# Kernel optimization log

Hardware: AMD Instinct MI355X
Metric: run time of the kernel (lower is better)

## Reference

```python
import jax, jax.numpy as jnp
import numpy as np

C = 256
G = min(C // 4, 32)  # GroupNorm groups = 32
EPS = 1e-6


def group_norm(x, gamma, beta):
    B, Cc, H, W = x.shape
    xg = x.reshape(B, G, Cc // G, H, W)
    mean = xg.mean(axis=(2, 3, 4), keepdims=True)
    var = xg.var(axis=(2, 3, 4), keepdims=True)
    xg = (xg - mean) / jnp.sqrt(var + EPS)
    x = xg.reshape(B, Cc, H, W)
    return x * gamma[None, :, None, None] + beta[None, :, None, None]


def nin(h, W_, b_):
    # 1x1 conv as channel contraction: [B,C,H,W] x [C,D] -> [B,D,H,W]
    return jnp.einsum('bchw,cd->bdhw', h, W_) + b_[None, :, None, None]


def setup_inputs() -> dict:
    key = jax.random.key(0)
    ks = jax.random.split(key, 12)
    B, H, Wd = 4, 64, 64
    x = jax.random.normal(ks[0], (B, C, H, Wd), dtype=jnp.float32)
    gn_gamma = jnp.ones((C,), jnp.float32)
    gn_beta = jnp.zeros((C,), jnp.float32)
    scale = 0.1
    w0 = jax.random.normal(ks[1], (C, C), jnp.float32) * scale
    b0 = jnp.zeros((C,), jnp.float32)
    w1 = jax.random.normal(ks[2], (C, C), jnp.float32) * scale
    b1 = jnp.zeros((C,), jnp.float32)
    w2 = jax.random.normal(ks[3], (C, C), jnp.float32) * scale
    b2 = jnp.zeros((C,), jnp.float32)
    w3 = jax.random.normal(ks[4], (C, C), jnp.float32) * scale
    b3 = jnp.zeros((C,), jnp.float32)
    return {"x": x, "gn_gamma": gn_gamma, "gn_beta": gn_beta,
            "w0": w0, "b0": b0, "w1": w1, "b1": b1,
            "w2": w2, "b2": b2, "w3": w3, "b3": b3}


def reference(x, gn_gamma, gn_beta, w0, b0, w1, b1, w2, b2, w3, b3):
    B, Cc, H, Wd = x.shape
    h = group_norm(x, gn_gamma, gn_beta)
    q = nin(h, w0, b0)
    k = nin(h, w1, b1)
    v = nin(h, w2, b2)
    # attention over all spatial positions; scores [B,H,W,H,W]
    w = jnp.einsum('bchw,bcij->bhwij', q, k) * (Cc ** -0.5)
    w = jax.nn.softmax(w.reshape(B, H, Wd, H * Wd), axis=-1)
    w = w.reshape(B, H, Wd, H, Wd)
    h = jnp.einsum('bhwij,bcij->bchw', w, v)
    h = nin(h, w3, b3)
    return x + h  # skip_rescale=False
```

## Files before the change

kernel.cpp:

```cpp
#include <hip/hip_runtime.h>
#include <math.h>


typedef short short8    __attribute__((ext_vector_type(8)));
typedef ushort ushort8  __attribute__((ext_vector_type(8)));
typedef ushort ushort4v __attribute__((ext_vector_type(4)));
typedef float f32x4     __attribute__((ext_vector_type(4)));
typedef float f32x16    __attribute__((ext_vector_type(16)));

#define BB 4
#define CCH 256
#define NSP 4096
#define TEN ((size_t)BB * NSP * CCH)

__device__ __forceinline__ float b2f(ushort h){
  unsigned int u = ((unsigned int)h) << 16;
  float f; __builtin_memcpy(&f, &u, 4); return f;
}
__device__ __forceinline__ ushort f2b(float f){
  unsigned int u; __builtin_memcpy(&u, &f, 4);
  u += 0x7fffu + ((u >> 16) & 1u);
  return (ushort)(u >> 16);
}
__device__ __forceinline__ unsigned int pk2(float a, float b){
  unsigned int r;
  asm("v_cvt_pk_bf16_f32 %0, %1, %2" : "=&v"(r) : "v"(a), "v"(b));
  return r;
}
__device__ __forceinline__ void dma16(const void* g, void* l){
  __builtin_amdgcn_global_load_lds((const __attribute__((address_space(1))) void*)g,
                                   (__attribute__((address_space(3))) void*)l,
                                   16, 0, 0);
}

__global__ __launch_bounds__(256) void pre_k(const float* __restrict__ x,
                                             const float* __restrict__ w0,
                                             const float* __restrict__ w1,
                                             const float* __restrict__ w2,
                                             const float* __restrict__ w3,
                                             ushort* __restrict__ wT,
                                             float* __restrict__ sums){
  __shared__ ushort tile[64][72];
  __shared__ float red[8];
  const int bxx = blockIdx.x;
  const int t = threadIdx.x;
  if (bxx < 64){
    const int wsel = bxx >> 4, tb = bxx & 15;
    const float* w = (wsel==0) ? w0 : (wsel==1) ? w1 : (wsel==2) ? w2 : w3;
    ushort* dst = wT + (size_t)wsel * 65536;
    const int r0 = (tb >> 2) * 64, c0 = (tb & 3) * 64;
    #pragma unroll
    for (int p = 0; p < 2; p++){
      const int r = p*32 + (t >> 3), cc = (t & 7)*8;
      const float* wr = w + (size_t)(r0 + r)*256 + c0 + cc;
      f32x4 a = *(const f32x4*)wr;
      f32x4 d = *(const f32x4*)(wr + 4);
      #pragma unroll
      for (int j = 0; j < 4; j++){
        tile[r][cc + j]     = f2b(a[j]);
        tile[r][cc + 4 + j] = f2b(d[j]);
      }
    }
    __syncthreads();
    #pragma unroll
    for (int p = 0; p < 2; p++){
      const int r = p*32 + (t >> 3), cc = (t & 7)*8;
      ushort8 ov;
      #pragma unroll
      for (int j = 0; j < 8; j++) ov[j] = tile[cc + j][r];
      *(ushort8*)(dst + (size_t)(c0 + r)*256 + r0 + cc) = ov;
    }
  } else {
    const int q = bxx - 64;
    const f32x4* p = (const f32x4*)(x + (size_t)(q >> 1)*32768 + (size_t)(q & 1)*16384);
    float s = 0.f, s2 = 0.f;
    for (int i = t; i < 4096; i += 256){
      f32x4 v = p[i];
      #pragma unroll
      for (int j = 0; j < 4; j++){ s += v[j]; s2 += v[j]*v[j]; }
    }
    #pragma unroll
    for (int off = 32; off >= 1; off >>= 1){
      s  += __shfl_down(s,  off, 64);
      s2 += __shfl_down(s2, off, 64);
    }
    const int w = t >> 6;
    if ((t & 63) == 0){ red[w*2] = s; red[w*2+1] = s2; }
    __syncthreads();
    if (t == 0){
      sums[q*2]   = red[0]+red[2]+red[4]+red[6];
      sums[q*2+1] = red[1]+red[3]+red[5]+red[7];
    }
  }
}

__global__ __launch_bounds__(256) void gn_apply_k(const float* __restrict__ x,
                                                  const float* __restrict__ sums,
                                                  const float* __restrict__ gamma,
                                                  const float* __restrict__ beta,
                                                  ushort* __restrict__ h_t){
  __shared__ ushort tile[64][72];
  const int b = blockIdx.z, c0 = blockIdx.y*64, n0 = blockIdx.x*64;
  const int t = threadIdx.x;
  #pragma unroll
  for (int p = 0; p < 2; p++){
    const int cl = p*32 + (t >> 3);
    const int nc = (t & 7) * 8;
    const int c = c0 + cl;
    const int bg = b*32 + (c>>3);
    const float S  = sums[bg*4+0] + sums[bg*4+2];
    const float S2 = sums[bg*4+1] + sums[bg*4+3];
    const float mean = S * (1.f/32768.f);
    const float rstd = rsqrtf(fmaxf(S2*(1.f/32768.f) - mean*mean, 0.f) + 1e-6f);
    const float sc = rstd * gamma[c];
    const float sh = beta[c] - mean * sc;
    const float* xr = x + ((size_t)b*CCH + c)*NSP + n0 + nc;
    f32x4 a = *(const f32x4*)xr;
    f32x4 d = *(const f32x4*)(xr + 4);
    #pragma unroll
    for (int j = 0; j < 4; j++){
      tile[nc + j][cl]     = f2b(a[j]*sc + sh);
      tile[nc + 4 + j][cl] = f2b(d[j]*sc + sh);
    }
  }
  __syncthreads();
  #pragma unroll
  for (int p = 0; p < 2; p++){
    const int nl = p*32 + (t >> 3);
    const int cc = (t & 7) * 8;
    ushort8 ov;
    #pragma unroll
    for (int j = 0; j < 8; j++) ov[j] = tile[nl][cc + j];
    *(ushort8*)(h_t + ((size_t)b*NSP + n0 + nl)*CCH + c0 + cc) = ov;
  }
}

__global__ __launch_bounds__(256) void gemm_qkv_k(const ushort* __restrict__ wT,
                                                  const ushort* __restrict__ h_t,
                                                  ushort* __restrict__ q_t,
                                                  ushort* __restrict__ k_t,
                                                  ushort* __restrict__ vout,
                                                  const float* __restrict__ b0,
                                                  const float* __restrict__ b1,
                                                  const float* __restrict__ b2){
  __shared__ ushort Bt[64*256];
  const int K = 256;
  const long HS = (long)NSP * CCH;
  const int t = threadIdx.x, w = t >> 6, lane = t & 63;
  const int li = lane & 15, quad = lane >> 4;
  const int batch = blockIdx.y;

  if (blockIdx.z == 0){
    const ushort* Bm = h_t + (size_t)batch * HS;
    ushort* out0 = q_t + (size_t)batch * HS;
    ushort* out1 = k_t + (size_t)batch * HS;
    const int nb = blockIdx.x * 64;

    #pragma unroll
    for (int i = 0; i < 8; i++){
      const int id = t + 256*i;
      const int row = id >> 5, gg = id & 31;
      *(ushort8*)&Bt[row*256 + (gg ^ (row & 31))*8] =
        *(const ushort8*)(Bm + (size_t)(nb + row)*K + gg*8);
    }
    __syncthreads();

    for (int tm = 0; tm < 4; tm++){
      const int m0 = tm*64 + w*16;
      short8 afr0[8], afr1[8];
      #pragma unroll
      for (int kk = 0; kk < 8; kk++){
        afr0[kk] = *(const short8*)(wT +         (size_t)(m0 + li)*K + kk*32 + quad*8);
        afr1[kk] = *(const short8*)(wT + 65536 + (size_t)(m0 + li)*K + kk*32 + quad*8);
      }
      #pragma unroll
      for (int nt = 0; nt < 4; nt++){
        f32x4 acc0 = {0.f,0.f,0.f,0.f};
        f32x4 acc1 = {0.f,0.f,0.f,0.f};
        const int n = nb + nt*16 + li;
        const int rowl = nt*16 + li;
        #pragma unroll
        for (int kk = 0; kk < 8; kk++){
          short8 bfr = *(const short8*)&Bt[rowl*256 + ((4*kk + quad) ^ (rowl & 31))*8];
          acc0 = __builtin_amdgcn_mfma_f32_16x16x32_bf16(afr0[kk], bfr, acc0, 0, 0, 0);
          acc1 = __builtin_amdgcn_mfma_f32_16x16x32_bf16(afr1[kk], bfr, acc1, 0, 0, 0);
        }
        float e0[4], e1[4];
        #pragma unroll
        for (int r2 = 0; r2 < 4; r2++){
          e0[r2] = acc0[r2] + b0[m0 + quad*4 + r2];
          e1[r2] = acc1[r2] + b1[m0 + quad*4 + r2];
        }
        uint2 d0; d0.x = pk2(e0[0], e0[1]); d0.y = pk2(e0[2], e0[3]);
        uint2 d1; d1.x = pk2(e1[0], e1[1]); d1.y = pk2(e1[2], e1[3]);
        const int m = m0 + quad*4;
        *(uint2*)(out0 + (size_t)n*256 + m) = d0;
        *(uint2*)(out1 + (size_t)(n >> 5)*8192 + (m >> 3)*256
                       + (n & 31)*8 + (m & 7)) = d1;
      }
    }
  } else {
    const ushort* A  = h_t + (size_t)batch * HS;
    const ushort* Bm = wT + 2*65536;
    ushort* OutT = vout + (size_t)batch * HS;
    const int m0 = blockIdx.x*64 + w*16;

    short8 afr[8];
    #pragma unroll
    for (int kk = 0; kk < 8; kk++)
      afr[kk] = *(const short8*)(A + (size_t)(m0 + li)*K + kk*32 + quad*8);

    for (int tn = 0; tn < 4; tn++){
      const int nb = tn*64;
      __syncthreads();
      #pragma unroll
      for (int i = 0; i < 8; i++){
        const int id = t + 256*i;
        const int row = id >> 5, gg = id & 31;
        *(ushort8*)&Bt[row*256 + (gg ^ (row & 31))*8] =
          *(const ushort8*)(Bm + (size_t)(nb + row)*K + gg*8);
      }
      __syncthreads();

      #pragma unroll
      for (int nt = 0; nt < 4; nt++){
        f32x4 acc = {0.f,0.f,0.f,0.f};
        const int n = nb + nt*16 + li;
        const int rowl = nt*16 + li;
        #pragma unroll
        for (int kk = 0; kk < 8; kk++){
          short8 bfr = *(const short8*)&Bt[rowl*256 + ((4*kk + quad) ^ (rowl & 31))*8];
          acc = __builtin_amdgcn_mfma_f32_16x16x32_bf16(afr[kk], bfr, acc, 0, 0, 0);
        }
        const float bn = b2[n];
        float e[4];
        #pragma unroll
        for (int r2 = 0; r2 < 4; r2++) e[r2] = acc[r2] + bn;
        uint2 dv; dv.x = pk2(e[0], e[1]); dv.y = pk2(e[2], e[3]);
        const int m = m0 + quad*4;
        *(uint2*)(OutT + (size_t)(m >> 5)*8192 + ((m >> 3) & 3)*2048
                       + (size_t)n*8 + (m & 7)) = dv;
      }
    }
  }
}

#define STAGE_KV(KDST, VDST, TILE)                                              \
  _Pragma("unroll")                                                             \
  for (int i_ = 0; i_ < 4; i_++){                                               \
    const int cell_ = (w*4 + i_)*64 + lane;                                     \
    dma16(kb + (size_t)(TILE)*8192 + cell_*8, &(KDST)[(w*4 + i_)*512]);         \
    dma16(vb + (size_t)(TILE)*8192 + cell_*8, &(VDST)[(w*4 + i_)*512]);         \
  }

#define ATTN_STEP(KC, VC, KN, VN, IT)                                           \
  {                                                                             \
    const int it_ = (IT);                                                       \
    const bool more_ = (it_ + 1 < iters);                                       \
    if (more_){                                                                 \
      STAGE_KV(KN, VN, tile0 + it_ + 1);                                        \
    }                                                                           \
    f32x16 sacc = (f32x16)(0.f);                                                \
    _Pragma("unroll")                                                           \
    for (int st = 0; st < 16; st++){                                            \
      short8 kf = *(const short8*)&(KC)[((st*2 + h)*32 + cl)*8];                \
      sacc = __builtin_amdgcn_mfma_f32_32x32x16_bf16(kf, qf[st], sacc, 0, 0, 0);\
    }                                                                           \
    unsigned int grp[4][2];                                                     \
    _Pragma("unroll")                                                           \
    for (int m = 0; m < 4; m++){                                                \
      float p0 = __builtin_amdgcn_exp2f(fminf(sacc[4*m+0]*c1 - M2, 30.f));      \
      float p1 = __builtin_amdgcn_exp2f(fminf(sacc[4*m+1]*c1 - M2, 30.f));      \
      float p2 = __builtin_amdgcn_exp2f(fminf(sacc[4*m+2]*c1 - M2, 30.f));      \
      float p3 = __builtin_amdgcn_exp2f(fminf(sacc[4*m+3]*c1 - M2, 30.f));      \
      l_i += (p0 + p1) + (p2 + p3);                                             \
      grp[m][0] = pk2(p0, p1);                                                  \
      grp[m][1] = pk2(p2, p3);                                                  \
    }                                                                           \
    unsigned int sa0 = h ? grp[0][0] : grp[1][0];                               \
    unsigned int sa1 = h ? grp[0][1] : grp[1][1];                               \
    unsigned int sb0 = h ? grp[2][0] : grp[3][0];                               \
    unsigned int sb1 = h ? grp[2][1] : grp[3][1];                               \
    unsigned int ra0 = __shfl_xor((int)sa0, 32, 64);                            \
    unsigned int ra1 = __shfl_xor((int)sa1, 32, 64);                            \
    unsigned int rb0 = __shfl_xor((int)sb0, 32, 64);                            \
    unsigned int rb1 = __shfl_xor((int)sb1, 32, 64);                            \
    unsigned int f0[4], f1[4];                                                  \
    if (h == 0){                                                                \
      f0[0]=grp[0][0]; f0[1]=grp[0][1]; f0[2]=ra0; f0[3]=ra1;                   \
      f1[0]=grp[2][0]; f1[1]=grp[2][1]; f1[2]=rb0; f1[3]=rb1;                   \
    } else {                                                                    \
      f0[0]=ra0; f0[1]=ra1; f0[2]=grp[1][0]; f0[3]=grp[1][1];                   \
      f1[0]=rb0; f1[1]=rb1; f1[2]=grp[3][0]; f1[3]=grp[3][1];                   \
    }                                                                           \
    short8 pf0, pf1;                                                            \
    __builtin_memcpy(&pf0, f0, 16);                                             \
    __builtin_memcpy(&pf1, f1, 16);                                             \
    _Pragma("unroll")                                                           \
    for (int ct = 0; ct < 8; ct++){                                             \
      short8 v0 = *(const short8*)&(VC)[(h*256 + ct*32 + cl)*8];                \
      short8 v1 = *(const short8*)&(VC)[((2 + h)*256 + ct*32 + cl)*8];          \
      oacc[ct] = __builtin_amdgcn_mfma_f32_32x32x16_bf16(pf0, v0, oacc[ct], 0, 0, 0); \
      oacc[ct] = __builtin_amdgcn_mfma_f32_32x32x16_bf16(pf1, v1, oacc[ct], 0, 0, 0); \
    }                                                                           \
    if (more_) __syncthreads();                                                 \
  }

__global__ __launch_bounds__(256, 2) void attn32_k(const ushort* __restrict__ qg,
                                                   const ushort* __restrict__ kg,
                                                   const ushort* __restrict__ vg,
                                                   ushort* __restrict__ ph01,
                                                   ushort* __restrict__ ph23,
                                                   float* __restrict__ lbuf,
                                                   int iters, int ks4){
  __shared__ ushort KtA[8192], KtB[8192];
  __shared__ ushort VtA[8192], VtB[8192];

  const int t = threadIdx.x, lane = t & 63;
  const int cl = lane & 31, h = lane >> 5;
  const int bx = blockIdx.x;
  const int qt = bx / ks4;
  const int r  = bx % ks4;
  const int s  = r >> 2, b = r & 3;
  const int n0 = qt * 128;
  const int w = t >> 6;
  const int qb = n0 + w*32;
  const int keybase = s * (iters * 32);
  const int tile0 = keybase >> 5;

  const ushort* kb = kg + (size_t)b*NSP*CCH;
  const ushort* vb = vg + (size_t)b*CCH*NSP;

  short8 qf[16];
  {
    const ushort* qrow = qg + ((size_t)b*NSP + qb + cl)*CCH + h*8;
    #pragma unroll
    for (int st = 0; st < 16; st++) qf[st] = *(const short8*)(qrow + st*16);
  }

  f32x16 oacc[8];
  #pragma unroll
  for (int i = 0; i < 8; i++) oacc[i] = (f32x16)(0.f);
  float l_i = 0.f;
  const float c1 = 0.0625f * 1.44269504088896f;
  const float M2 = 24.f;

  STAGE_KV(KtA, VtA, tile0);
  __syncthreads();

  for (int it = 0; it < iters; it += 2){
    ATTN_STEP(KtA, VtA, KtB, VtB, it);
    ATTN_STEP(KtB, VtB, KtA, VtA, it + 1);
  }

  ushort* ps = (s < 2) ? (ph01 + (size_t)s*TEN) : (ph23 + (size_t)(s-2)*TEN);
  ps += (size_t)b * NSP * CCH;
  #pragma unroll
  for (int ct = 0; ct < 8; ct++){
    const size_t crow = (size_t)(ct*32 + cl) * NSP;
    #pragma unroll
    for (int m = 0; m < 4; m++){
      unsigned int d0 = pk2(oacc[ct][4*m+0], oacc[ct][4*m+1]);
      unsigned int d1 = pk2(oacc[ct][4*m+2], oacc[ct][4*m+3]);
      uint2 dv; dv.x = d0; dv.y = d1;
      *(uint2*)(ps + crow + qb + 8*m + 4*h) = dv;
    }
  }
  l_i += __shfl_xor(l_i, 32, 64);
  if (h == 0)
    lbuf[(size_t)s*BB*NSP + (size_t)b*NSP + qb + cl] = l_i;
}

__global__ __launch_bounds__(256) void combine_k(const ushort* __restrict__ ph01,
                                                 const ushort* __restrict__ ph23,
                                                 const float* __restrict__ lbuf,
                                                 ushort* __restrict__ Oc, int ks){
  __shared__ ushort T[64*66];
  const int t = threadIdx.x;
  const int q0 = blockIdx.x * 64, c0 = blockIdx.y * 64, b = blockIdx.z;
  const int ql4 = (t & 15) * 4;
  const int cs  = t >> 4;
  float rl[4];
  #pragma unroll
  for (int j = 0; j < 4; j++){
    float suml = 0.f;
    for (int sp = 0; sp < ks; sp++)
      suml += lbuf[(size_t)sp*BB*NSP + (size_t)b*NSP + q0 + ql4 + j];
    rl[j] = 1.f / suml;
  }
  #pragma unroll
  for (int ci = 0; ci < 4; ci++){
    const int c = cs*4 + ci;
    float acc[4] = {0.f, 0.f, 0.f, 0.f};
    for (int sp = 0; sp < ks; sp++){
      const ushort* pp = (sp < 2) ? (ph01 + (size_t)sp*TEN) : (ph23 + (size_t)(sp-2)*TEN);
      ushort4v u = *(const ushort4v*)(pp + ((size_t)b*CCH + c0 + c)*NSP + q0 + ql4);
      #pragma unroll
      for (int j = 0; j < 4; j++) acc[j] += b2f(u[j]);
    }
    #pragma unroll
    for (int j = 0; j < 4; j++)
      T[(ql4 + j)*66 + c] = f2b(acc[j] * rl[j]);
  }
  __syncthreads();
  const int q2 = t >> 2, ch = (t & 3) * 16;
  ushort8 o0, o1;
  #pragma unroll
  for (int j = 0; j < 8; j++){ o0[j] = T[q2*66 + ch + j]; o1[j] = T[q2*66 + ch + 8 + j]; }
  ushort* dst = Oc + ((size_t)b*NSP + q0 + q2)*CCH + c0 + ch;
  *(ushort8*)dst = o0;
  *(ushort8*)(dst + 8) = o1;
}

__global__ __launch_bounds__(256) void gemm_proj_k(const ushort* __restrict__ A,
                                                   const ushort* __restrict__ Bm,
                                                   const float* __restrict__ b3,
                                                   const float* __restrict__ xin,
                                                   float* __restrict__ out){
  __shared__ ushort Bt[64*256];
  const int K = 256;
  const int t = threadIdx.x, w = t >> 6, lane = t & 63;
  const int li = lane & 15, quad = lane >> 4;
  const int tm = blockIdx.x & 63, tn = blockIdx.x >> 6;
  const int batch = blockIdx.y;
  A   += (size_t)batch * NSP * CCH;
  xin += (size_t)batch * CCH * NSP;
  out += (size_t)batch * CCH * NSP;
  const int m0 = tm*64 + w*16;
  const int nb = tn*64;

  #pragma unroll
  for (int i = 0; i < 8; i++){
    const int id = t + 256*i;
    const int row = id >> 5, gg = id & 31;
    *(ushort8*)&Bt[row*256 + (gg ^ (row & 31))*8] =
      *(const ushort8*)(Bm + (size_t)(nb + row)*K + gg*8);
  }
  short8 afr[8];
  #pragma unroll
  for (int kk = 0; kk < 8; kk++)
    afr[kk] = *(const short8*)(A + (size_t)(m0 + li)*K + kk*32 + quad*8);
  __syncthreads();

  #pragma unroll
  for (int nt = 0; nt < 4; nt++){
    f32x4 acc = {0.f,0.f,0.f,0.f};
    const int d = nb + nt*16 + li;
    const int rowl = nt*16 + li;
    #pragma unroll
    for (int kk = 0; kk < 8; kk++){
      short8 bfr = *(const short8*)&Bt[rowl*256 + ((4*kk + quad) ^ (rowl & 31))*8];
      acc = __builtin_amdgcn_mfma_f32_16x16x32_bf16(afr[kk], bfr, acc, 0, 0, 0);
    }
    const float bias = b3[d];
    const size_t idx = (size_t)d*NSP + m0 + quad*4;
    f32x4 xv = *(const f32x4*)(xin + idx);
    f32x4 ov;
    #pragma unroll
    for (int r = 0; r < 4; r++) ov[r] = acc[r] + bias + xv[r];
    *(f32x4*)(out + idx) = ov;
  }
}

extern "C" void kernel_launch(void* const* d_in, const int* in_sizes, int n_in,
                              void* d_out, int out_size, void* d_ws, size_t ws_size,
                              hipStream_t stream){
  const float* x     = (const float*)d_in[0];
  const float* gamma = (const float*)d_in[1];
  const float* beta  = (const float*)d_in[2];
  const float* w0    = (const float*)d_in[3];
  const float* b0    = (const float*)d_in[4];
  const float* w1    = (const float*)d_in[5];
  const float* b1    = (const float*)d_in[6];
  const float* w2    = (const float*)d_in[7];
  const float* b2    = (const float*)d_in[8];
  const float* w3    = (const float*)d_in[9];
  const float* b3    = (const float*)d_in[10];
  float* out = (float*)d_out;

  ushort* h_t  = (ushort*)d_out;
  ushort* ph01 = (ushort*)d_out;
  ushort* q_t = (ushort*)d_ws;
  ushort* k_t = q_t + TEN;
  ushort* v   = k_t + TEN;
  ushort* wT  = v + TEN;
  float* sums  = (float*)(wT + 4*65536);
  float* lbuf  = sums + 512;
  ushort* ph23 = (ushort*)(lbuf + 4*BB*NSP);

  const size_t need4 = ((3*TEN + 4*65536)*2) + (512 + 4*BB*NSP)*4 + 2*TEN*2;
  const int ks = (ws_size >= need4) ? 4 : 2;
  const int iters = NSP / (ks * 32);

  pre_k<<<dim3(320), 256, 0, stream>>>(x, w0, w1, w2, w3, wT, sums);
  gn_apply_k<<<dim3(64,4,4), 256, 0, stream>>>(x, sums, gamma, beta, h_t);
  gemm_qkv_k<<<dim3(64, BB, 2), 256, 0, stream>>>(wT, h_t, q_t, k_t, v, b0, b1, b2);

  attn32_k<<<128*ks, 256, 0, stream>>>(q_t, k_t, v, ph01, ph23, lbuf, iters, 4*ks);

  ushort* Oc = k_t;
  combine_k<<<dim3(64, 4, BB), 256, 0, stream>>>(ph01, ph23, lbuf, Oc, ks);
  gemm_proj_k<<<dim3(256, BB), 256, 0, stream>>>(Oc, wT + 3*65536, b3, x, out);
}
```

Baseline: 216.3 us.

## Fuse split-K attention combine into output projection GEMM kernel

Adds a kernel that sums the split-K partial attention outputs, normalizes them by the summed softmax denominators, stages the result in shared memory and then runs the output 1x1 projection with MFMA plus bias and residual. This removes the separate combine kernel and the round trip of the combined tensor through global memory. It needs all partials placed in workspace rather than aliasing the output, so it only runs when the workspace is large enough, and it falls back to the old path otherwise. Each block reloads the full projection weight matrix for only 32 query positions, which adds weight traffic.

```diff
diff --git a/kernel.cpp b/kernel.cpp
--- a/kernel.cpp
+++ b/kernel.cpp
@@ -371,6 +371,89 @@
     lbuf[(size_t)s*BB*NSP + (size_t)b*NSP + qb + cl] = l_i;
 }
 
+__global__ __launch_bounds__(256) void proj_comb_k(const ushort* __restrict__ ph01,
+                                                   const ushort* __restrict__ ph23,
+                                                   const float* __restrict__ lbuf,
+                                                   const ushort* __restrict__ Bm,
+                                                   const float* __restrict__ b3,
+                                                   const float* __restrict__ xin,
+                                                   float* __restrict__ out, int ks){
+  __shared__ ushort At[32*256];
+  __shared__ ushort Bt[64*256];
+  const int K = 256;
+  const int t = threadIdx.x, w = t >> 6, lane = t & 63;
+  const int li = lane & 15, quad = lane >> 4;
+  const int q0 = blockIdx.x * 32, b = blockIdx.y;
+
+  const int ql4 = (t & 7) * 4;
+  const int cs  = t >> 3;
+  float rl[4];
+  #pragma unroll
+  for (int j = 0; j < 4; j++){
+    float suml = 0.f;
+    for (int sp = 0; sp < ks; sp++)
+      suml += lbuf[(size_t)sp*BB*NSP + (size_t)b*NSP + q0 + ql4 + j];
+    rl[j] = 1.f / suml;
+  }
+  #pragma unroll
+  for (int ci = 0; ci < 8; ci++){
+    const int c = cs*8 + ci;
+    float acc[4] = {0.f, 0.f, 0.f, 0.f};
+    for (int sp = 0; sp < ks; sp++){
+      const ushort* pp = (sp < 2) ? (ph01 + (size_t)sp*TEN) : (ph23 + (size_t)(sp-2)*TEN);
+      ushort4v u = *(const ushort4v*)(pp + ((size_t)b*CCH + c)*NSP + q0 + ql4);
+      #pragma unroll
+      for (int j = 0; j < 4; j++) acc[j] += b2f(u[j]);
+    }
+    const int g = c >> 3, co = c & 7;
+    #pragma unroll
+    for (int j = 0; j < 4; j++){
+      const int row = ql4 + j;
+      At[row*256 + ((g ^ row) & 31)*8 + co] = f2b(acc[j] * rl[j]);
+    }
+  }
+  __syncthreads();
+
+  const int mrow = (w & 1)*16 + li;
+  short8 afr[8];
+  #pragma unroll
+  for (int kk = 0; kk < 8; kk++)
+    afr[kk] = *(const short8*)&At[mrow*256 + (((4*kk + quad) ^ mrow) & 31)*8];
+
+  xin += (size_t)b * CCH * NSP;
+  out += (size_t)b * CCH * NSP;
+  for (int tn = 0; tn < 4; tn++){
+    __syncthreads();
+    #pragma unroll
+    for (int i = 0; i < 8; i++){
+      const int id = t + 256*i;
+      const int row = id >> 5, gg = id & 31;
+      *(ushort8*)&Bt[row*256 + (gg ^ (row & 31))*8] =
+        *(const ushort8*)(Bm + (size_t)(tn*64 + row)*K + gg*8);
+    }
+    __syncthreads();
+
+    #pragma unroll
+    for (int s2 = 0; s2 < 2; s2++){
+      f32x4 acc = {0.f,0.f,0.f,0.f};
+      const int rowb = (w >> 1)*32 + s2*16 + li;
+      const int d = tn*64 + rowb;
+      #pragma unroll
+      for (int kk = 0; kk < 8; kk++){
+        short8 bfr = *(const short8*)&Bt[rowb*256 + (((4*kk + quad) ^ rowb) & 31)*8];
+        acc = __builtin_amdgcn_mfma_f32_16x16x32_bf16(afr[kk], bfr, acc, 0, 0, 0);
+      }
+      const float bias = b3[d];
+      const size_t idx = (size_t)d*NSP + q0 + (w & 1)*16 + quad*4;
+      f32x4 xv = *(const f32x4*)(xin + idx);
+      f32x4 ov;
+      #pragma unroll
+      for (int r2 = 0; r2 < 4; r2++) ov[r2] = acc[r2] + bias + xv[r2];
+      *(f32x4*)(out + idx) = ov;
+    }
+  }
+}
+
 __global__ __launch_bounds__(256) void combine_k(const ushort* __restrict__ ph01,
                                                  const ushort* __restrict__ ph23,
                                                  const float* __restrict__ lbuf,
@@ -479,26 +562,34 @@
   float* out = (float*)d_out;
 
   ushort* h_t  = (ushort*)d_out;
-  ushort* ph01 = (ushort*)d_out;
   ushort* q_t = (ushort*)d_ws;
   ushort* k_t = q_t + TEN;
   ushort* v   = k_t + TEN;
   ushort* wT  = v + TEN;
   float* sums  = (float*)(wT + 4*65536);
   float* lbuf  = sums + 512;
-  ushort* ph23 = (ushort*)(lbuf + 4*BB*NSP);
+  ushort* phA = (ushort*)(lbuf + 4*BB*NSP);
+  ushort* phB = phA + 2*TEN;
 
   const size_t need4 = ((3*TEN + 4*65536)*2) + (512 + 4*BB*NSP)*4 + 2*TEN*2;
+  const size_t need5 = need4 + 2*TEN*2;
   const int ks = (ws_size >= need4) ? 4 : 2;
+  const int fused = (ws_size >= need5) && (ks == 4);
   const int iters = NSP / (ks * 32);
 
   pre_k<<<dim3(320), 256, 0, stream>>>(x, w0, w1, w2, w3, wT, sums);
   gn_apply_k<<<dim3(64,4,4), 256, 0, stream>>>(x, sums, gamma, beta, h_t);
   gemm_qkv_k<<<dim3(64, BB, 2), 256, 0, stream>>>(wT, h_t, q_t, k_t, v, b0, b1, b2);
 
-  attn32_k<<<128*ks, 256, 0, stream>>>(q_t, k_t, v, ph01, ph23, lbuf, iters, 4*ks);
-
-  ushort* Oc = k_t;
-  combine_k<<<dim3(64, 4, BB), 256, 0, stream>>>(ph01, ph23, lbuf, Oc, ks);
-  gemm_proj_k<<<dim3(256, BB), 256, 0, stream>>>(Oc, wT + 3*65536, b3, x, out);
-}
+  if (fused){
+    attn32_k<<<128*ks, 256, 0, stream>>>(q_t, k_t, v, phA, phB, lbuf, iters, 4*ks);
+    proj_comb_k<<<dim3(128, BB), 256, 0, stream>>>(phA, phB, lbuf,
+                                                   wT + 3*65536, b3, x, out, ks);
+  } else {
+    ushort* ph01 = (ushort*)d_out;
+    attn32_k<<<128*ks, 256, 0, stream>>>(q_t, k_t, v, ph01, phA, lbuf, iters, 4*ks);
+    ushort* Oc = k_t;
+    combine_k<<<dim3(64, 4, BB), 256, 0, stream>>>(ph01, phA, lbuf, Oc, ks);
+    gemm_proj_k<<<dim3(256, BB), 256, 0, stream>>>(Oc, wT + 3*65536, b3, x, out);
+  }
+}
```

Result: faster. 210.7 us (-2.6%).
